# Optimization experiments

Hardware: AMD Instinct MI355X
Metric: run time of the kernel (lower is better)

## Reference

```python
import jax, jax.numpy as jnp
import numpy as np

SCALE = 1.0
P0 = 0.1


def setup_inputs() -> dict:
    key = jax.random.key(0)
    k1, k2, k3, k4 = jax.random.split(key, 4)
    B, N, D, T, TM = 64, 2048, 128, 512, 512
    data = jax.random.normal(k1, (B, N, D), dtype=jnp.float32)
    targets = jax.random.normal(k2, (B, N), dtype=jnp.float32)
    W = jax.random.normal(k3, (D, T), dtype=jnp.float32)        # major task pool, (n_dims, n_tasks)
    W_minor = jax.random.normal(k4, (D, TM), dtype=jnp.float32)  # minor task pool
    return {"data": data, "targets": targets, "W": W, "W_minor": W_minor}


def reference(data, targets, W, W_minor):
    # data: (B, N, D); targets: (B, N); W: (D, T); W_minor: (D, TM)
    n_minor = W_minor.shape[1]
    W_all = jnp.concatenate([W, W_minor], axis=1)            # (D, T_total)
    XW = jnp.einsum('bnd,dt->bnt', data, W_all)              # (B, N, T_total)
    diff2 = (targets[..., None] - XW) ** 2                   # (B, N, T_total)
    # Prefix sum-of-squared-residuals: step i uses points 0..i-1 (step 0 -> zeros,
    # matching the original's zeros-prefix call).
    prefix = jnp.cumsum(diff2, axis=1)
    prefix = jnp.concatenate([jnp.zeros_like(prefix[:, :1]), prefix[:, :-1]], axis=1)
    # Log priors: original hardcodes log((1-p0)/3) for major tasks (kept faithfully).
    log_prior_major = float(np.log((1.0 - P0) / 3.0))
    log_prior_minor = float(np.log(P0 / n_minor))
    log_prior = jnp.concatenate([
        jnp.full((W.shape[1],), log_prior_major, dtype=data.dtype),
        jnp.full((n_minor,), log_prior_minor, dtype=data.dtype),
    ])                                                        # (T_total,)
    log_probs = -0.5 * prefix / (SCALE ** 2) + log_prior      # (B, N, T_total)
    weights = jax.nn.softmax(log_probs, axis=-1)              # posterior over tasks
    w_mmse = jnp.einsum('bnt,dt->bnd', weights, W_all)        # (B, N, D)
    preds = jnp.sum(data * w_mmse, axis=-1)                   # (B, N)
    return preds
```

## Files before the change

### kernel.cpp

```cpp
#include <hip/hip_runtime.h>

typedef _Float16 half8 __attribute__((ext_vector_type(8)));
typedef float floatx4 __attribute__((ext_vector_type(4)));

#define NB 64
#define NN 2048
#define ND 128
#define NT 1024
#define NC 16
#define NCHUNKS 128

#define ALPHA 0.84932184f
#define INV_ALPHA 1.17741002f
#define LP2_MAJOR (-1.7369655941662063f)
#define LP2_MINOR (-12.321928094887362f)

__device__ __forceinline__ float fexp2(float x) {
  float r;
  asm("v_exp_f32 %0, %1" : "=v"(r) : "v"(x));
  return r;
}

#define PIN8(x) asm volatile("" : "+v"(x))

template <int CTRL>
__device__ __forceinline__ float dppshr_add(float x) {
  int i = __builtin_bit_cast(int, x);
  int s = __builtin_amdgcn_update_dpp(0, i, CTRL, 0xF, 0xF, true);
  return x + __builtin_bit_cast(float, s);
}
__device__ __forceinline__ float scan16(float x) {
  x = dppshr_add<0x111>(x);
  x = dppshr_add<0x112>(x);
  x = dppshr_add<0x114>(x);
  x = dppshr_add<0x118>(x);
  return x;
}
__device__ __forceinline__ float bcast15(float x) {
  int i = __builtin_bit_cast(int, x);
  i = __builtin_amdgcn_ds_swizzle(i, 0x1F0);
  return __builtin_bit_cast(float, i);
}

__global__ void k_prep(const float* __restrict__ W, const float* __restrict__ Wm,
                       _Float16* __restrict__ Wph, _Float16* __restrict__ Wpl) {
  int idx = blockIdx.x * 256 + threadIdx.x;
  int t = idx >> 7, d = idx & 127;
  float x = (t < 512) ? W[d * 512 + t] : Wm[d * 512 + (t - 512)];
  x *= ALPHA;
  _Float16 h = (_Float16)x;
  _Float16 l = (_Float16)(x - (float)h);
  Wph[idx] = h;
  Wpl[idx] = l;
}

__global__ void k_prep_data(const float* __restrict__ data,
                            _Float16* __restrict__ Apk) {
  int idx = blockIdx.x * 256 + threadIdx.x;
  int l = idx & 63, kk = (idx >> 6) & 3, ch = (idx >> 8) & 127, b = idx >> 15;
  int row = ch * 16 + (l & 15);
  int dcol = kk * 32 + (l >> 4) * 8;
  const float* src = data + ((size_t)b * NN + row) * ND + dcol;
  floatx4 a0 = *(const floatx4*)src;
  floatx4 a1 = *(const floatx4*)(src + 4);
  half8 h, lo;
#pragma unroll
  for (int j = 0; j < 4; ++j) {
    h[j] = (_Float16)a0[j];
    lo[j] = (_Float16)(a0[j] - (float)h[j]);
    h[4 + j] = (_Float16)a1[j];
    lo[4 + j] = (_Float16)(a1[j] - (float)h[4 + j]);
  }
  size_t o = ((size_t)(b * 128 + ch)) * 4096 + kk * 512 + l * 8;
  *(half8*)(Apk + o) = h;
  *(half8*)(Apk + o + 2048) = lo;
}

__global__ __launch_bounds__(512, 4)
void k_fused(const _Float16* __restrict__ Apk, const float* __restrict__ targets,
             const _Float16* __restrict__ Wph, const _Float16* __restrict__ Wpl,
             floatx4* __restrict__ part) {
  int bid = blockIdx.x;
  int xcd = bid & 7, rest = bid >> 3;
  int tq = rest & 7, b = (rest >> 3) * 8 + xcd;
  int tid = threadIdx.x;
  int w = tid >> 6, l = tid & 63;
  int l15 = l & 15, lhi = l >> 4;
  int wavebase = tq * 128 + w * 16;

  half8 wh[4], wl[4];
#pragma unroll
  for (int kk = 0; kk < 4; ++kk) {
    int off = (wavebase + l15) * 128 + kk * 32 + lhi * 8;
    wh[kk] = *(const half8*)(Wph + off);
    wl[kk] = *(const half8*)(Wpl + off);
  }
#pragma unroll
  for (int kk = 0; kk < 4; ++kk) { PIN8(wh[kk]); PIN8(wl[kk]); }

  float prior2 = (tq < 4) ? LP2_MAJOR : LP2_MINOR;
  float run[4] = {0.f, 0.f, 0.f, 0.f};

  const _Float16* abase = Apk + (size_t)b * 128 * 4096;
  const float* tgp = targets + (size_t)b * NN + l15;
  size_t pbase = (size_t)b * NN * 8 + tq;

  __shared__ _Float16 Abuf[2][4096];
  __shared__ float sm[8][4][4][16][4];

  int wslot = w * 512 + l * 8;

  half8 stg = *(const half8*)(abase + wslot);
  *(half8*)&Abuf[0][wslot] = stg;
  stg = *(const half8*)(abase + 4096 + wslot);
  __syncthreads();

  for (int ch = 0; ch < NCHUNKS; ++ch) {
    int cur = ch & 1;
    half8 ah[4], al[4];
#pragma unroll
    for (int kk = 0; kk < 4; ++kk) {
      ah[kk] = *(const half8*)&Abuf[cur][kk * 512 + l * 8];
      al[kk] = *(const half8*)&Abuf[cur][2048 + kk * 512 + l * 8];
    }
    floatx4 acc = {0.f, 0.f, 0.f, 0.f};
#pragma unroll
    for (int kk = 0; kk < 4; ++kk) {
      acc = __builtin_amdgcn_mfma_f32_16x16x32_f16(wh[kk], ah[kk], acc, 0, 0, 0);
      acc = __builtin_amdgcn_mfma_f32_16x16x32_f16(wh[kk], al[kk], acc, 0, 0, 0);
      acc = __builtin_amdgcn_mfma_f32_16x16x32_f16(wl[kk], ah[kk], acc, 0, 0, 0);
    }
    float tgs = tgp[0] * ALPHA;

    float q[4], inc[4], lp[4];
#pragma unroll
    for (int r = 0; r < 4; ++r) {
      float d = tgs - acc[r];
      q[r] = d * d;
    }
#pragma unroll
    for (int r = 0; r < 4; ++r)
      inc[r] = scan16(q[r]);
#pragma unroll
    for (int r = 0; r < 4; ++r)
      lp[r] = (prior2 - run[r]) + (q[r] - inc[r]);
#pragma unroll
    for (int r = 0; r < 4; ++r)
      run[r] += bcast15(inc[r]);

    float m = fmaxf(fmaxf(lp[0], lp[1]), fmaxf(lp[2], lp[3]));
    float s1 = 0.f, s2 = 0.f;
#pragma unroll
    for (int r = 0; r < 4; ++r) {
      float e = fexp2(lp[r] - m);
      s1 += e;
      s2 = fmaf(e, acc[r], s2);
    }
    sm[w][ch & 3][lhi][l15][0] = m;
    sm[w][ch & 3][lhi][l15][1] = s1;
    sm[w][ch & 3][lhi][l15][2] = s2;

    *(half8*)&Abuf[cur ^ 1][wslot] = stg;
    int pf = (ch + 2 < NCHUNKS) ? ch + 2 : NCHUNKS - 1;
    stg = *(const half8*)(abase + (size_t)pf * 4096 + wslot);

    if ((ch & 3) == 3) {
      __syncthreads();
      if (tid < 64) {
        int c4 = tid >> 4, row = tid & 15;
        float M = -3.4e38f;
#pragma unroll
        for (int wv = 0; wv < 8; ++wv)
#pragma unroll
          for (int g = 0; g < 4; ++g)
            M = fmaxf(M, sm[wv][c4][g][row][0]);
        float S1 = 0.f, S2 = 0.f;
#pragma unroll
        for (int wv = 0; wv < 8; ++wv)
#pragma unroll
          for (int g = 0; g < 4; ++g) {
            float e = fexp2(sm[wv][c4][g][row][0] - M);
            S1 = fmaf(sm[wv][c4][g][row][1], e, S1);
            S2 = fmaf(sm[wv][c4][g][row][2], e, S2);
          }
        floatx4 v;
        v[0] = M; v[1] = S1; v[2] = S2; v[3] = 0.f;
        part[pbase + (size_t)((ch - 3 + c4) * 16 + row) * 8] = v;
      }
    }
    __syncthreads();
    tgp += NC;
  }
}

__global__ void k_combine(const floatx4* __restrict__ part, float* __restrict__ out) {
  int idx = blockIdx.x * 256 + threadIdx.x;
  const floatx4* p = part + (size_t)idx * 8;
  floatx4 v[8];
  float M = -3.4e38f;
#pragma unroll
  for (int j = 0; j < 8; ++j) { v[j] = p[j]; M = fmaxf(M, v[j][0]); }
  float s1 = 0.f, s2 = 0.f;
#pragma unroll
  for (int j = 0; j < 8; ++j) {
    float e = fexp2(v[j][0] - M);
    s1 += v[j][1] * e;
    s2 += v[j][2] * e;
  }
  out[idx] = s2 / s1 * INV_ALPHA;
}

extern "C" void kernel_launch(void* const* d_in, const int* in_sizes, int n_in,
                              void* d_out, int out_size, void* d_ws, size_t ws_size,
                              hipStream_t stream) {
  const float* data    = (const float*)d_in[0];
  const float* targets = (const float*)d_in[1];
  const float* W       = (const float*)d_in[2];
  const float* Wm      = (const float*)d_in[3];
  float* out = (float*)d_out;

  char* ws = (char*)d_ws;
  const size_t MB = 1u << 20;
  _Float16* Wph  = (_Float16*)ws;
  _Float16* Wpl  = (_Float16*)(ws + 256 * 1024);
  _Float16* Apk  = (_Float16*)(ws + 512 * 1024);
  floatx4* part  = (floatx4*)(ws + 512 * 1024 + 64 * MB);

  k_prep<<<512, 256, 0, stream>>>(W, Wm, Wph, Wpl);
  k_prep_data<<<8192, 256, 0, stream>>>(data, Apk);
  k_fused<<<NB * 8, 512, 0, stream>>>(Apk, targets, Wph, Wpl, part);
  k_combine<<<(NB * NN) / 256, 256, 0, stream>>>(part, out);
}
```

Baseline: 195.4 us.

## Process two chunks per iteration with split MFMA accumulators and padded LDS

The main loop now handles two 16-row chunks per iteration, with a double-buffered LDS tile holding a pair of chunks. The three hi/lo MFMA products go into independent accumulators, which breaks the serial MFMA dependency chain. This halves the number of block-wide barriers and raises instruction-level parallelism. The reduction scratch is re-laid out with padding to reduce LDS bank conflicts. In exchange, LDS and register use grow, which may lower occupancy per CU.

```diff
diff --git a/kernel.cpp b/kernel.cpp
--- a/kernel.cpp
+++ b/kernel.cpp
@@ -9,6 +9,7 @@
 #define NT 1024
 #define NC 16
 #define NCHUNKS 128
+#define NIV 64
 
 #define ALPHA 0.84932184f
 #define INV_ALPHA 1.17741002f
@@ -105,66 +106,93 @@
   const float* tgp = targets + (size_t)b * NN + l15;
   size_t pbase = (size_t)b * NN * 8 + tq;
 
-  __shared__ _Float16 Abuf[2][4096];
-  __shared__ float sm[8][4][4][16][4];
+  __shared__ _Float16 Abuf[2][2][4096];
+  __shared__ float sm[8][4][65][3];
 
   int wslot = w * 512 + l * 8;
 
-  half8 stg = *(const half8*)(abase + wslot);
-  *(half8*)&Abuf[0][wslot] = stg;
-  stg = *(const half8*)(abase + 4096 + wslot);
+#define EPI(ACC, SLOT, TGOFF)                                         \
+  do {                                                                \
+    float tgs = tgp[TGOFF] * ALPHA;                                   \
+    float q[4], inc[4], lp[4];                                        \
+    _Pragma("unroll")                                                 \
+    for (int r = 0; r < 4; ++r) {                                     \
+      float d = tgs - ACC[r];                                         \
+      q[r] = d * d;                                                   \
+    }                                                                 \
+    _Pragma("unroll")                                                 \
+    for (int r = 0; r < 4; ++r) inc[r] = scan16(q[r]);                \
+    _Pragma("unroll")                                                 \
+    for (int r = 0; r < 4; ++r)                                       \
+      lp[r] = (prior2 - run[r]) + (q[r] - inc[r]);                    \
+    _Pragma("unroll")                                                 \
+    for (int r = 0; r < 4; ++r) run[r] += bcast15(inc[r]);            \
+    float m = fmaxf(fmaxf(lp[0], lp[1]), fmaxf(lp[2], lp[3]));        \
+    float s1 = 0.f, s2 = 0.f;                                         \
+    _Pragma("unroll")                                                 \
+    for (int r = 0; r < 4; ++r) {                                     \
+      float e = fexp2(lp[r] - m);                                     \
+      s1 += e;                                                        \
+      s2 = fmaf(e, ACC[r], s2);                                       \
+    }                                                                 \
+    sm[w][SLOT][l][0] = m;                                            \
+    sm[w][SLOT][l][1] = s1;                                           \
+    sm[w][SLOT][l][2] = s2;                                           \
+  } while (0)
+
+#define GEMM3(ACC, AH, AL)                                                        \
+  do {                                                                            \
+    floatx4 hh = {0.f, 0.f, 0.f, 0.f};                                            \
+    floatx4 hl = {0.f, 0.f, 0.f, 0.f};                                            \
+    floatx4 lh = {0.f, 0.f, 0.f, 0.f};                                            \
+    _Pragma("unroll")                                                             \
+    for (int kk = 0; kk < 4; ++kk) {                                              \
+      hh = __builtin_amdgcn_mfma_f32_16x16x32_f16(wh[kk], AH[kk], hh, 0, 0, 0);   \
+      hl = __builtin_amdgcn_mfma_f32_16x16x32_f16(wh[kk], AL[kk], hl, 0, 0, 0);   \
+      lh = __builtin_amdgcn_mfma_f32_16x16x32_f16(wl[kk], AH[kk], lh, 0, 0, 0);   \
+    }                                                                             \
+    ACC = (hh + hl) + lh;                                                         \
+  } while (0)
+
+  half8 s0 = *(const half8*)(abase + wslot);
+  half8 s1 = *(const half8*)(abase + 4096 + wslot);
+  *(half8*)&Abuf[0][0][wslot] = s0;
+  *(half8*)&Abuf[0][1][wslot] = s1;
+  s0 = *(const half8*)(abase + 2 * 4096 + wslot);
+  s1 = *(const half8*)(abase + 3 * 4096 + wslot);
   __syncthreads();
 
-  for (int ch = 0; ch < NCHUNKS; ++ch) {
-    int cur = ch & 1;
-    half8 ah[4], al[4];
+  for (int iv = 0; iv < NIV; ++iv) {
+    int cur = iv & 1;
+    half8 ahA[4], alA[4];
 #pragma unroll
     for (int kk = 0; kk < 4; ++kk) {
-      ah[kk] = *(const half8*)&Abuf[cur][kk * 512 + l * 8];
-      al[kk] = *(const half8*)&Abuf[cur][2048 + kk * 512 + l * 8];
+      ahA[kk] = *(const half8*)&Abuf[cur][0][kk * 512 + l * 8];
+      alA[kk] = *(const half8*)&Abuf[cur][0][2048 + kk * 512 + l * 8];
     }
-    floatx4 acc = {0.f, 0.f, 0.f, 0.f};
+    floatx4 accA;
+    GEMM3(accA, ahA, alA);
+    half8 ahB[4], alB[4];
 #pragma unroll
     for (int kk = 0; kk < 4; ++kk) {
-      acc = __builtin_amdgcn_mfma_f32_16x16x32_f16(wh[kk], ah[kk], acc, 0, 0, 0);
-      acc = __builtin_amdgcn_mfma_f32_16x16x32_f16(wh[kk], al[kk], acc, 0, 0, 0);
-      acc = __builtin_amdgcn_mfma_f32_16x16x32_f16(wl[kk], ah[kk], acc, 0, 0, 0);
+      ahB[kk] = *(const half8*)&Abuf[cur][1][kk * 512 + l * 8];
+      alB[kk] = *(const half8*)&Abuf[cur][1][2048 + kk * 512 + l * 8];
     }
-    float tgs = tgp[0] * ALPHA;
-
-    float q[4], inc[4], lp[4];
-#pragma unroll
-    for (int r = 0; r < 4; ++r) {
-      float d = tgs - acc[r];
-      q[r] = d * d;
-    }
-#pragma unroll
-    for (int r = 0; r < 4; ++r)
-      inc[r] = scan16(q[r]);
-#pragma unroll
-    for (int r = 0; r < 4; ++r)
-      lp[r] = (prior2 - run[r]) + (q[r] - inc[r]);
-#pragma unroll
-    for (int r = 0; r < 4; ++r)
-      run[r] += bcast15(inc[r]);
-
-    float m = fmaxf(fmaxf(lp[0], lp[1]), fmaxf(lp[2], lp[3]));
-    float s1 = 0.f, s2 = 0.f;
-#pragma unroll
-    for (int r = 0; r < 4; ++r) {
-      float e = fexp2(lp[r] - m);
-      s1 += e;
-      s2 = fmaf(e, acc[r], s2);
-    }
-    sm[w][ch & 3][lhi][l15][0] = m;
-    sm[w][ch & 3][lhi][l15][1] = s1;
-    sm[w][ch & 3][lhi][l15][2] = s2;
-
-    *(half8*)&Abuf[cur ^ 1][wslot] = stg;
-    int pf = (ch + 2 < NCHUNKS) ? ch + 2 : NCHUNKS - 1;
-    stg = *(const half8*)(abase + (size_t)pf * 4096 + wslot);
-
-    if ((ch & 3) == 3) {
+    floatx4 accB;
+    GEMM3(accB, ahB, alB);
+
+    *(half8*)&Abuf[cur ^ 1][0][wslot] = s0;
+    *(half8*)&Abuf[cur ^ 1][1][wslot] = s1;
+    int pfA = 2 * iv + 4, pfB = 2 * iv + 5;
+    pfA = pfA > 127 ? 127 : pfA;
+    pfB = pfB > 127 ? 127 : pfB;
+    s0 = *(const half8*)(abase + (size_t)pfA * 4096 + wslot);
+    s1 = *(const half8*)(abase + (size_t)pfB * 4096 + wslot);
+
+    EPI(accA, ((2 * iv) & 3), 0);
+    EPI(accB, ((2 * iv + 1) & 3), 16);
+
+    if (iv & 1) {
       __syncthreads();
       if (tid < 64) {
         int c4 = tid >> 4, row = tid & 15;
@@ -173,24 +201,26 @@
         for (int wv = 0; wv < 8; ++wv)
 #pragma unroll
           for (int g = 0; g < 4; ++g)
-            M = fmaxf(M, sm[wv][c4][g][row][0]);
+            M = fmaxf(M, sm[wv][c4][g * 16 + row][0]);
         float S1 = 0.f, S2 = 0.f;
 #pragma unroll
         for (int wv = 0; wv < 8; ++wv)
 #pragma unroll
           for (int g = 0; g < 4; ++g) {
-            float e = fexp2(sm[wv][c4][g][row][0] - M);
-            S1 = fmaf(sm[wv][c4][g][row][1], e, S1);
-            S2 = fmaf(sm[wv][c4][g][row][2], e, S2);
+            float e = fexp2(sm[wv][c4][g * 16 + row][0] - M);
+            S1 = fmaf(sm[wv][c4][g * 16 + row][1], e, S1);
+            S2 = fmaf(sm[wv][c4][g * 16 + row][2], e, S2);
           }
         floatx4 v;
         v[0] = M; v[1] = S1; v[2] = S2; v[3] = 0.f;
-        part[pbase + (size_t)((ch - 3 + c4) * 16 + row) * 8] = v;
+        part[pbase + (size_t)((2 * iv - 2 + c4) * 16 + row) * 8] = v;
       }
     }
     __syncthreads();
-    tgp += NC;
-  }
+    tgp += 32;
+  }
+#undef EPI
+#undef GEMM3
 }
 
 __global__ void k_combine(const floatx4* __restrict__ part, float* __restrict__ out) {
```

Result: faster. 182.3 us (-6.7%).
